# Kernel optimization log

Hardware: AMD Instinct MI355X
Metric: run time of the kernel (lower is better)

Reference implementation:

```python
import jax, jax.numpy as jnp
import numpy as np

N = 100000   # num_nodes
E = 3200000  # num_edges
F = 7        # node_features
H = 128      # hidden_dim
D = 64       # embedding_dim
EPS = 1e-5


def setup_inputs() -> dict:
    key = jax.random.key(0)
    ks = jax.random.split(key, 32)
    inp = {}
    inp["x"] = jax.random.normal(ks[0], (N, F), jnp.float32)
    inp["edge_index"] = jax.random.randint(ks[1], (2, E), 0, N, dtype=jnp.int64)
    # input projection
    inp["W_in"] = jax.random.normal(ks[2], (F, H), jnp.float32) * 0.1
    inp["b_in"] = jax.random.normal(ks[3], (H,), jnp.float32) * 0.01
    # 3 GCN layers: 128->128, 128->128, 128->64, each with eval-mode BatchNorm params
    dims = [(H, H), (H, H), (H, D)]
    for i, (di, do) in enumerate(dims):
        k = jax.random.split(ks[4 + i], 6)
        inp[f"W{i}"] = jax.random.normal(k[0], (di, do), jnp.float32) * (1.0 / np.sqrt(di))
        inp[f"b{i}"] = jax.random.normal(k[1], (do,), jnp.float32) * 0.01
        inp[f"g{i}"] = 1.0 + 0.1 * jax.random.normal(k[2], (do,), jnp.float32)
        inp[f"be{i}"] = 0.1 * jax.random.normal(k[3], (do,), jnp.float32)
        inp[f"m{i}"] = 0.1 * jax.random.normal(k[4], (do,), jnp.float32)
        inp[f"v{i}"] = jax.random.uniform(k[5], (do,), jnp.float32, 0.5, 1.5)
    return inp


def _gcn_conv(x, W, b, src, dst, dinv):
    h = x @ W                                   # [N, do]
    coef = dinv[src] * dinv[dst]                # [E]
    agg = jax.ops.segment_sum(h[src] * coef[:, None], dst, num_segments=N)
    # self-loop contribution: norm = dinv[i]^2
    return agg + h * (dinv * dinv)[:, None] + b


def _bn_eval(x, g, be, m, v):
    return (x - m) * (g * jax.lax.rsqrt(v + EPS)) + be


def reference(x, edge_index, W_in, b_in,
              W0, b0, g0, be0, m0, v0,
              W1, b1, g1, be1, m1, v1,
              W2, b2, g2, be2, m2, v2):
    src, dst = edge_index[0], edge_index[1]
    # in-degree with self-loops (same for all layers)
    deg = jax.ops.segment_sum(jnp.ones((E,), x.dtype), dst, num_segments=N) + 1.0
    dinv = jax.lax.rsqrt(deg)

    h = jax.nn.relu(x @ W_in + b_in)            # [N, H]

    # layer 0: conv -> bn -> relu -> (dropout=id, eval) -> residual
    h0 = _gcn_conv(h, W0, b0, src, dst, dinv)
    h0 = jax.nn.relu(_bn_eval(h0, g0, be0, m0, v0)) + h
    # layer 1
    h1 = _gcn_conv(h0, W1, b1, src, dst, dinv)
    h1 = jax.nn.relu(_bn_eval(h1, g1, be1, m1, v1)) + h0
    # layer 2 (final): conv -> bn only (shape changes to D, no residual/relu)
    h2 = _gcn_conv(h1, W2, b2, src, dst, dinv)
    return _bn_eval(h2, g2, be2, m2, v2)        # [N, D]
```

## Files before the change

kernel.cpp:

```cpp
#include <hip/hip_runtime.h>


#define NN 100000
#define NE 3200000
#define FI 7
#define HD 128
#define DD 64
#define EPS 1e-5f
#define NB 196
#define EPB 8192
#define NBLK ((NE + EPB - 1) / EPB)
#define EMAX 20000

typedef float float2v __attribute__((ext_vector_type(2)));
typedef short short8 __attribute__((ext_vector_type(8)));
typedef float f32x4 __attribute__((ext_vector_type(4)));

__device__ __forceinline__ unsigned char f2fp8(float f) {
    return (unsigned char)(__builtin_amdgcn_cvt_pk_fp8_f32(f, f, 0, false) & 0xFF);
}
__device__ __forceinline__ unsigned short f2bf(float f) {
    unsigned u = __float_as_uint(f);
    u += 0x7FFF + ((u >> 16) & 1);
    return (unsigned short)(u >> 16);
}


__global__ __launch_bounds__(256) void pA_bin(const int* __restrict__ ei,
                                              int* __restrict__ bcnt,
                                              int* __restrict__ ebin) {
    __shared__ int sdst[EPB];
    __shared__ int hcur[NB];
    const int t = threadIdx.x;
    for (int b = t; b < NB; b += 256) hcur[b] = 0;
    __syncthreads();
    const int base = blockIdx.x * EPB;
    const int cnt = min(EPB, NE - base);
    for (int i = t; i < cnt; i += 256) {
        int d = ei[NE + base + i];
        sdst[i] = d;
        atomicAdd(&hcur[d >> 9], 1);
    }
    __syncthreads();
    for (int b = t; b < NB; b += 256) {
        int c = hcur[b];
        hcur[b] = (c ? atomicAdd(&bcnt[b], c) : 0) + b * EMAX;
    }
    __syncthreads();
    for (int i = t; i < cnt; i += 256) {
        int s = ei[base + i];
        int d = sdst[i];
        int p = atomicAdd(&hcur[d >> 9], 1);
        ebin[p] = ((d & 511) << 23) | s;
    }
}

__global__ __launch_bounds__(512) void p4_finalize(const int* __restrict__ bcnt,
                                                   const int* __restrict__ ebin,
                                                   int* __restrict__ esrc,
                                                   int* __restrict__ rowstart,
                                                   float* __restrict__ dinv) {
    __shared__ int sh[256];
    __shared__ int lh[512];
    __shared__ int sc[512];
    __shared__ int lc[512];
    const int t = threadIdx.x;
    const int b = blockIdx.x;
    if (t < 256) sh[t] = (t < NB) ? bcnt[t] : 0;
    __syncthreads();
    for (int off = 1; off < 256; off <<= 1) {
        int v = (t < 256 && t >= off) ? sh[t - off] : 0;
        __syncthreads();
        if (t < 256) sh[t] += v;
        __syncthreads();
    }
    const int ecnt = bcnt[b];
    const int ebase = sh[b] - ecnt;
    const int rbase = b * EMAX;
    const int n0 = b << 9;
    lh[t] = 0;
    __syncthreads();
    for (int i = t; i < ecnt; i += 512)
        atomicAdd(&lh[((unsigned)ebin[rbase + i]) >> 23], 1);
    __syncthreads();
    const int c = lh[t];
    sc[t] = c;
    __syncthreads();
    for (int off = 1; off < 512; off <<= 1) {
        int v = (t >= off) ? sc[t - off] : 0;
        __syncthreads();
        sc[t] += v;
        __syncthreads();
    }
    const int excl = ebase + sc[t] - c;
    lc[t] = excl;
    const int node = n0 + t;
    if (node < NN) {
        rowstart[node] = excl;
        dinv[node] = rsqrtf((float)c + 1.0f);
    }
    if (b == NB - 1 && t == 0) rowstart[NN] = NE;
    __syncthreads();
    for (int i = t; i < ecnt; i += 512) {
        int v = ebin[rbase + i];
        int p = atomicAdd(&lc[((unsigned)v) >> 23], 1);
        esrc[p] = v & 0x7FFFFF;
    }
}


__global__ __launch_bounds__(256) void inproj_kernel(const float* __restrict__ x,
                                                     const float* __restrict__ W_in,
                                                     const float* __restrict__ b_in,
                                                     float* __restrict__ hA,
                                                     unsigned short* __restrict__ hAbf) {
    int n = blockIdx.x * 2 + (threadIdx.x >> 7);
    int j = threadIdx.x & 127;
    float acc = b_in[j];
#pragma unroll
    for (int f = 0; f < FI; ++f) acc += x[n * FI + f] * W_in[f * HD + j];
    acc = fmaxf(acc, 0.f);
    hA[n * HD + j] = acc;
    hAbf[n * HD + j] = f2bf(acc);
}


__global__ __launch_bounds__(64) void wprep_all(const float* __restrict__ W0,
                                                const float* __restrict__ W1,
                                                const float* __restrict__ W2,
                                                unsigned short* __restrict__ wf0,
                                                unsigned short* __restrict__ wf1,
                                                unsigned short* __restrict__ wf2) {
    const int blk = blockIdx.x;
    const float* W;
    unsigned short* Wf;
    int DO, rel;
    if (blk < 32) { W = W0; Wf = wf0; DO = 128; rel = blk; }
    else if (blk < 64) { W = W1; Wf = wf1; DO = 128; rel = blk - 32; }
    else { W = W2; Wf = wf2; DO = 64; rel = blk - 64; }
    const int lane = threadIdx.x;
    const int nt = rel >> 2;
    const int ks = rel & 3;
    short8 o;
#pragma unroll
    for (int j = 0; j < 8; ++j)
        o[j] = (short)f2bf(W[(ks * 32 + (lane >> 4) * 8 + j) * DO + nt * 16 + (lane & 15)]);
    *(short8*)(Wf + ((size_t)rel * 64 + lane) * 8) = o;
}


template <int DO>
__global__ __launch_bounds__(256) void gemm_mfma(const unsigned short* __restrict__ A,
                                                 const unsigned short* __restrict__ Wf,
                                                 const float* __restrict__ dinv,
                                                 unsigned char* __restrict__ B) {
    constexpr int CT = DO / 64;
    const int tid = threadIdx.x;
    const int wave = tid >> 6;
    const int lane = tid & 63;
    const int n0 = blockIdx.x * 32;
    short8 bfrag[CT][4];
#pragma unroll
    for (int ct = 0; ct < CT; ++ct)
#pragma unroll
        for (int ks = 0; ks < 4; ++ks)
            bfrag[ct][ks] = *(const short8*)(Wf + ((size_t)(((wave * CT + ct) * 4 + ks) * 64) + lane) * 8);
#pragma unroll
    for (int rt = 0; rt < 2; ++rt) {
        const int arow = n0 + rt * 16 + (lane & 15);
        short8 afrag[4];
#pragma unroll
        for (int ks = 0; ks < 4; ++ks)
            afrag[ks] = *(const short8*)(A + (size_t)arow * HD + ks * 32 + ((lane >> 4) & 3) * 8);
        f32x4 acc[CT];
#pragma unroll
        for (int ct = 0; ct < CT; ++ct) acc[ct] = (f32x4){0.f, 0.f, 0.f, 0.f};
#pragma unroll
        for (int ks = 0; ks < 4; ++ks)
#pragma unroll
            for (int ct = 0; ct < CT; ++ct)
                acc[ct] = __builtin_amdgcn_mfma_f32_16x16x32_bf16(afrag[ks], bfrag[ct][ks], acc[ct], 0, 0, 0);
#pragma unroll
        for (int r = 0; r < 4; ++r) {
            const int orow = n0 + rt * 16 + (lane >> 4) * 4 + r;
            const float dv = dinv[orow];
#pragma unroll
            for (int ct = 0; ct < CT; ++ct) {
                const int ocol = (wave * CT + ct) * 16 + (lane & 15);
                B[(size_t)orow * DO + ocol] = f2fp8(acc[ct][r] * dv);
            }
        }
    }
}


template <int DO, bool RELU_RES>
__global__ __launch_bounds__(128) void gather_kernel(const unsigned char* __restrict__ hXW,
                                                     float* __restrict__ resOut,
                                                     unsigned short* __restrict__ resBf,
                                                     const int* __restrict__ rowstart,
                                                     const int* __restrict__ esrc,
                                                     const float* __restrict__ dinv,
                                                     const float* __restrict__ bias,
                                                     const float* __restrict__ g,
                                                     const float* __restrict__ be,
                                                     const float* __restrict__ m,
                                                     const float* __restrict__ v) {
    constexpr int CG = DO / 8;
    constexpr int NG = 128 / CG;
    constexpr int QN = DO / 4;
    __shared__ int s_idx[128];
    __shared__ float sred[8][128];
    const int n = blockIdx.x;
    const int t = threadIdx.x;
    const int rs = rowstart[n];
    const int re = rowstart[n + 1];
    const float dn = dinv[n];
    const int q = t & (CG - 1);
    const int grp = t / CG;
    float4 a0l = {0.f, 0.f, 0.f, 0.f}, a0h = {0.f, 0.f, 0.f, 0.f};
    float4 a1l = {0.f, 0.f, 0.f, 0.f}, a1h = {0.f, 0.f, 0.f, 0.f};
    for (int base = rs; base < re; base += 128) {
        const int c = min(128, re - base);
        __syncthreads();
        if (t < c) s_idx[t] = esrc[base + t];
        __syncthreads();
        for (int j = grp; j < c; j += 2 * NG) {
            {
                const uint2 u = *(const uint2*)(hXW + (size_t)s_idx[j] * DO + q * 8);
                const float2v l0 = __builtin_amdgcn_cvt_pk_f32_fp8(u.x, false);
                const float2v h0 = __builtin_amdgcn_cvt_pk_f32_fp8(u.x, true);
                const float2v l1 = __builtin_amdgcn_cvt_pk_f32_fp8(u.y, false);
                const float2v h1 = __builtin_amdgcn_cvt_pk_f32_fp8(u.y, true);
                a0l.x += l0.x; a0l.y += l0.y; a0l.z += h0.x; a0l.w += h0.y;
                a0h.x += l1.x; a0h.y += l1.y; a0h.z += h1.x; a0h.w += h1.y;
            }
            if (j + NG < c) {
                const uint2 u = *(const uint2*)(hXW + (size_t)s_idx[j + NG] * DO + q * 8);
                const float2v l0 = __builtin_amdgcn_cvt_pk_f32_fp8(u.x, false);
                const float2v h0 = __builtin_amdgcn_cvt_pk_f32_fp8(u.x, true);
                const float2v l1 = __builtin_amdgcn_cvt_pk_f32_fp8(u.y, false);
                const float2v h1 = __builtin_amdgcn_cvt_pk_f32_fp8(u.y, true);
                a1l.x += l0.x; a1l.y += l0.y; a1l.z += h0.x; a1l.w += h0.y;
                a1h.x += l1.x; a1h.y += l1.y; a1h.z += h1.x; a1h.w += h1.y;
            }
        }
    }
    a0l.x += a1l.x; a0l.y += a1l.y; a0l.z += a1l.z; a0l.w += a1l.w;
    a0h.x += a1h.x; a0h.y += a1h.y; a0h.z += a1h.z; a0h.w += a1h.w;
    __syncthreads();
    sred[0][t] = a0l.x; sred[1][t] = a0l.y; sred[2][t] = a0l.z; sred[3][t] = a0l.w;
    sred[4][t] = a0h.x; sred[5][t] = a0h.y; sred[6][t] = a0h.z; sred[7][t] = a0h.w;
    __syncthreads();
    if (t < QN) {
        const int qq = t >> 1, h = t & 1;
        float4 sum = {0.f, 0.f, 0.f, 0.f};
#pragma unroll
        for (int k = 0; k < NG; ++k) {
            const int u = k * CG + qq;
            sum.x += sred[h * 4 + 0][u];
            sum.y += sred[h * 4 + 1][u];
            sum.z += sred[h * 4 + 2][u];
            sum.w += sred[h * 4 + 3][u];
        }
        const unsigned su = *(const unsigned*)(hXW + (size_t)n * DO + t * 4);
        const float2v slo = __builtin_amdgcn_cvt_pk_f32_fp8(su, false);
        const float2v shi = __builtin_amdgcn_cvt_pk_f32_fp8(su, true);
        const float4 b4 = *(const float4*)(bias + t * 4);
        const float4 g4 = *(const float4*)(g + t * 4);
        const float4 be4 = *(const float4*)(be + t * 4);
        const float4 m4 = *(const float4*)(m + t * 4);
        const float4 v4 = *(const float4*)(v + t * 4);
        float4 val;
        val.x = (sum.x + slo.x) * dn + b4.x;
        val.y = (sum.y + slo.y) * dn + b4.y;
        val.z = (sum.z + shi.x) * dn + b4.z;
        val.w = (sum.w + shi.y) * dn + b4.w;
        val.x = (val.x - m4.x) * (g4.x * rsqrtf(v4.x + EPS)) + be4.x;
        val.y = (val.y - m4.y) * (g4.y * rsqrtf(v4.y + EPS)) + be4.y;
        val.z = (val.z - m4.z) * (g4.z * rsqrtf(v4.z + EPS)) + be4.z;
        val.w = (val.w - m4.w) * (g4.w * rsqrtf(v4.w + EPS)) + be4.w;
        float4* outp = (float4*)(resOut + (size_t)n * DO + t * 4);
        if (RELU_RES) {
            const float4 r = *outp;
            val.x = fmaxf(val.x, 0.f) + r.x;
            val.y = fmaxf(val.y, 0.f) + r.y;
            val.z = fmaxf(val.z, 0.f) + r.z;
            val.w = fmaxf(val.w, 0.f) + r.w;
            ushort4 bf;
            bf.x = f2bf(val.x); bf.y = f2bf(val.y);
            bf.z = f2bf(val.z); bf.w = f2bf(val.w);
            *(ushort4*)(resBf + (size_t)n * DO + t * 4) = bf;
        }
        *outp = val;
    }
}


extern "C" void kernel_launch(void* const* d_in, const int* in_sizes, int n_in,
                              void* d_out, int out_size, void* d_ws, size_t ws_size,
                              hipStream_t stream) {
    const float* x    = (const float*)d_in[0];
    const int*   ei   = (const int*)d_in[1];
    const float* W_in = (const float*)d_in[2];
    const float* b_in = (const float*)d_in[3];
    const float* Wl[3] = {(const float*)d_in[4], (const float*)d_in[10], (const float*)d_in[16]};
    const float* bl[3] = {(const float*)d_in[5], (const float*)d_in[11], (const float*)d_in[17]};
    const float* gl[3] = {(const float*)d_in[6], (const float*)d_in[12], (const float*)d_in[18]};
    const float* bel[3] = {(const float*)d_in[7], (const float*)d_in[13], (const float*)d_in[19]};
    const float* ml[3] = {(const float*)d_in[8], (const float*)d_in[14], (const float*)d_in[20]};
    const float* vl[3] = {(const float*)d_in[9], (const float*)d_in[15], (const float*)d_in[21]};
    float* out = (float*)d_out;

    char* ws = (char*)d_ws;
    size_t off = 0;
    auto carve = [&](size_t bytes) {
        void* p = ws + off;
        off += (bytes + 255) & ~(size_t)255;
        return p;
    };
    int*   bcnt     = (int*)carve(NB * sizeof(int));
    int*   rowstart = (int*)carve((NN + 1) * sizeof(int));
    float* dinv     = (float*)carve(NN * sizeof(float));
    int*   esrc     = (int*)carve((size_t)NE * sizeof(int));
    float* hA       = (float*)carve((size_t)NN * HD * sizeof(float));
    unsigned short* hAbf = (unsigned short*)carve((size_t)NN * HD * sizeof(unsigned short));
    unsigned char* hB = (unsigned char*)carve((size_t)NN * HD);
    int*   ebin     = (int*)carve((size_t)NB * EMAX * sizeof(int));
    unsigned short* wf0 = (unsigned short*)carve((size_t)HD * HD * sizeof(unsigned short));
    unsigned short* wf1 = (unsigned short*)carve((size_t)HD * HD * sizeof(unsigned short));
    unsigned short* wf2 = (unsigned short*)carve((size_t)HD * DD * sizeof(unsigned short));
    (void)ws_size;

    hipMemsetAsync(bcnt, 0, NB * sizeof(int), stream);

    wprep_all<<<80, 64, 0, stream>>>(Wl[0], Wl[1], Wl[2], wf0, wf1, wf2);

    pA_bin<<<NBLK, 256, 0, stream>>>(ei, bcnt, ebin);
    p4_finalize<<<NB, 512, 0, stream>>>(bcnt, ebin, esrc, rowstart, dinv);

    inproj_kernel<<<NN / 2, 256, 0, stream>>>(x, W_in, b_in, hA, hAbf);

    gemm_mfma<128><<<NN / 32, 256, 0, stream>>>(hAbf, wf0, dinv, hB);
    gather_kernel<128, true><<<NN, 128, 0, stream>>>(hB, hA, hAbf, rowstart, esrc, dinv,
                                                     bl[0], gl[0], bel[0], ml[0], vl[0]);
    gemm_mfma<128><<<NN / 32, 256, 0, stream>>>(hAbf, wf1, dinv, hB);
    gather_kernel<128, true><<<NN, 128, 0, stream>>>(hB, hA, hAbf, rowstart, esrc, dinv,
                                                     bl[1], gl[1], bel[1], ml[1], vl[1]);
    gemm_mfma<64><<<NN / 32, 256, 0, stream>>>(hAbf, wf2, dinv, hB);
    gather_kernel<64, false><<<NN, 128, 0, stream>>>(hB, out, (unsigned short*)nullptr,
                                                     rowstart, esrc, dinv,
                                                     bl[2], gl[2], bel[2], ml[2], vl[2]);
}
```

Measured before the change: 516.3 us.

## Map one destination node per wavefront in gather with shuffle reduction

The CSR gather kernel used to assign one 128-thread block per node, staging edge indices in shared memory and reducing partial sums through shared memory with several block barriers. It now assigns one 64-lane wavefront per node, four nodes per 256-thread block. Each lane reads edge indices straight from global memory, and the partial sums are combined with xor shuffles, so no LDS or __syncthreads is needed. This cuts barrier and launch overhead for the roughly 32-edge average degree. In exchange each node gets fewer lanes to work in parallel, and index loads are no longer coalesced through shared memory.

After: 555.5 us. +7.6%, slower.

```diff
diff --git a/kernel.cpp b/kernel.cpp
--- a/kernel.cpp
+++ b/kernel.cpp
@@ -194,105 +194,116 @@
 }
 
 
-template <int DO, bool RELU_RES>
-__global__ __launch_bounds__(128) void gather_kernel(const unsigned char* __restrict__ hXW,
-                                                     float* __restrict__ resOut,
-                                                     unsigned short* __restrict__ resBf,
-                                                     const int* __restrict__ rowstart,
-                                                     const int* __restrict__ esrc,
-                                                     const float* __restrict__ dinv,
-                                                     const float* __restrict__ bias,
-                                                     const float* __restrict__ g,
-                                                     const float* __restrict__ be,
-                                                     const float* __restrict__ m,
-                                                     const float* __restrict__ v) {
-    constexpr int CG = DO / 8;
-    constexpr int NG = 128 / CG;
-    constexpr int QN = DO / 4;
-    __shared__ int s_idx[128];
-    __shared__ float sred[8][128];
-    const int n = blockIdx.x;
+template <int DOS, bool RELU_RES>
+__global__ __launch_bounds__(256) void gather_wave(const unsigned char* __restrict__ hXW,
+                                                   float* __restrict__ resOut,
+                                                   unsigned short* __restrict__ resBf,
+                                                   const int* __restrict__ rowstart,
+                                                   const int* __restrict__ esrc,
+                                                   const float* __restrict__ dinv,
+                                                   const float* __restrict__ bias,
+                                                   const float* __restrict__ g,
+                                                   const float* __restrict__ be,
+                                                   const float* __restrict__ m,
+                                                   const float* __restrict__ v) {
+    constexpr int CG = DOS / 8;
+    constexpr int G = 64 / CG;
     const int t = threadIdx.x;
+    const int lane = t & 63;
+    const int n = blockIdx.x * 4 + (t >> 6);
     const int rs = rowstart[n];
     const int re = rowstart[n + 1];
-    const float dn = dinv[n];
-    const int q = t & (CG - 1);
-    const int grp = t / CG;
-    float4 a0l = {0.f, 0.f, 0.f, 0.f}, a0h = {0.f, 0.f, 0.f, 0.f};
-    float4 a1l = {0.f, 0.f, 0.f, 0.f}, a1h = {0.f, 0.f, 0.f, 0.f};
-    for (int base = rs; base < re; base += 128) {
-        const int c = min(128, re - base);
-        __syncthreads();
-        if (t < c) s_idx[t] = esrc[base + t];
-        __syncthreads();
-        for (int j = grp; j < c; j += 2 * NG) {
-            {
-                const uint2 u = *(const uint2*)(hXW + (size_t)s_idx[j] * DO + q * 8);
-                const float2v l0 = __builtin_amdgcn_cvt_pk_f32_fp8(u.x, false);
-                const float2v h0 = __builtin_amdgcn_cvt_pk_f32_fp8(u.x, true);
-                const float2v l1 = __builtin_amdgcn_cvt_pk_f32_fp8(u.y, false);
-                const float2v h1 = __builtin_amdgcn_cvt_pk_f32_fp8(u.y, true);
-                a0l.x += l0.x; a0l.y += l0.y; a0l.z += h0.x; a0l.w += h0.y;
-                a0h.x += l1.x; a0h.y += l1.y; a0h.z += h1.x; a0h.w += h1.y;
-            }
-            if (j + NG < c) {
-                const uint2 u = *(const uint2*)(hXW + (size_t)s_idx[j + NG] * DO + q * 8);
-                const float2v l0 = __builtin_amdgcn_cvt_pk_f32_fp8(u.x, false);
-                const float2v h0 = __builtin_amdgcn_cvt_pk_f32_fp8(u.x, true);
-                const float2v l1 = __builtin_amdgcn_cvt_pk_f32_fp8(u.y, false);
-                const float2v h1 = __builtin_amdgcn_cvt_pk_f32_fp8(u.y, true);
-                a1l.x += l0.x; a1l.y += l0.y; a1l.z += h0.x; a1l.w += h0.y;
-                a1h.x += l1.x; a1h.y += l1.y; a1h.z += h1.x; a1h.w += h1.y;
-            }
+    const int q = lane & (CG - 1);
+    const int grp = lane / CG;
+    float4 al = {0.f, 0.f, 0.f, 0.f}, ah = {0.f, 0.f, 0.f, 0.f};
+    float4 bl = {0.f, 0.f, 0.f, 0.f}, bh = {0.f, 0.f, 0.f, 0.f};
+    for (int j = rs + grp; j < re; j += 2 * G) {
+        {
+            const int idx = esrc[j];
+            const uint2 u = *(const uint2*)(hXW + (size_t)idx * DOS + q * 8);
+            const float2v l0 = __builtin_amdgcn_cvt_pk_f32_fp8(u.x, false);
+            const float2v h0 = __builtin_amdgcn_cvt_pk_f32_fp8(u.x, true);
+            const float2v l1 = __builtin_amdgcn_cvt_pk_f32_fp8(u.y, false);
+            const float2v h1 = __builtin_amdgcn_cvt_pk_f32_fp8(u.y, true);
+            al.x += l0.x; al.y += l0.y; al.z += h0.x; al.w += h0.y;
+            ah.x += l1.x; ah.y += l1.y; ah.z += h1.x; ah.w += h1.y;
         }
-    }
-    a0l.x += a1l.x; a0l.y += a1l.y; a0l.z += a1l.z; a0l.w += a1l.w;
-    a0h.x += a1h.x; a0h.y += a1h.y; a0h.z += a1h.z; a0h.w += a1h.w;
-    __syncthreads();
-    sred[0][t] = a0l.x; sred[1][t] = a0l.y; sred[2][t] = a0l.z; sred[3][t] = a0l.w;
-    sred[4][t] = a0h.x; sred[5][t] = a0h.y; sred[6][t] = a0h.z; sred[7][t] = a0h.w;
-    __syncthreads();
-    if (t < QN) {
-        const int qq = t >> 1, h = t & 1;
-        float4 sum = {0.f, 0.f, 0.f, 0.f};
-#pragma unroll
-        for (int k = 0; k < NG; ++k) {
-            const int u = k * CG + qq;
-            sum.x += sred[h * 4 + 0][u];
-            sum.y += sred[h * 4 + 1][u];
-            sum.z += sred[h * 4 + 2][u];
-            sum.w += sred[h * 4 + 3][u];
+        if (j + G < re) {
+            const int idx = esrc[j + G];
+            const uint2 u = *(const uint2*)(hXW + (size_t)idx * DOS + q * 8);
+            const float2v l0 = __builtin_amdgcn_cvt_pk_f32_fp8(u.x, false);
+            const float2v h0 = __builtin_amdgcn_cvt_pk_f32_fp8(u.x, true);
+            const float2v l1 = __builtin_amdgcn_cvt_pk_f32_fp8(u.y, false);
+            const float2v h1 = __builtin_amdgcn_cvt_pk_f32_fp8(u.y, true);
+            bl.x += l0.x; bl.y += l0.y; bl.z += h0.x; bl.w += h0.y;
+            bh.x += l1.x; bh.y += l1.y; bh.z += h1.x; bh.w += h1.y;
         }
-        const unsigned su = *(const unsigned*)(hXW + (size_t)n * DO + t * 4);
-        const float2v slo = __builtin_amdgcn_cvt_pk_f32_fp8(su, false);
-        const float2v shi = __builtin_amdgcn_cvt_pk_f32_fp8(su, true);
-        const float4 b4 = *(const float4*)(bias + t * 4);
-        const float4 g4 = *(const float4*)(g + t * 4);
-        const float4 be4 = *(const float4*)(be + t * 4);
-        const float4 m4 = *(const float4*)(m + t * 4);
-        const float4 v4 = *(const float4*)(v + t * 4);
-        float4 val;
-        val.x = (sum.x + slo.x) * dn + b4.x;
-        val.y = (sum.y + slo.y) * dn + b4.y;
-        val.z = (sum.z + shi.x) * dn + b4.z;
-        val.w = (sum.w + shi.y) * dn + b4.w;
-        val.x = (val.x - m4.x) * (g4.x * rsqrtf(v4.x + EPS)) + be4.x;
-        val.y = (val.y - m4.y) * (g4.y * rsqrtf(v4.y + EPS)) + be4.y;
-        val.z = (val.z - m4.z) * (g4.z * rsqrtf(v4.z + EPS)) + be4.z;
-        val.w = (val.w - m4.w) * (g4.w * rsqrtf(v4.w + EPS)) + be4.w;
-        float4* outp = (float4*)(resOut + (size_t)n * DO + t * 4);
+    }
+    al.x += bl.x; al.y += bl.y; al.z += bl.z; al.w += bl.w;
+    ah.x += bh.x; ah.y += bh.y; ah.z += bh.z; ah.w += bh.w;
+#pragma unroll
+    for (int mask = CG; mask < 64; mask <<= 1) {
+        al.x += __shfl_xor(al.x, mask); al.y += __shfl_xor(al.y, mask);
+        al.z += __shfl_xor(al.z, mask); al.w += __shfl_xor(al.w, mask);
+        ah.x += __shfl_xor(ah.x, mask); ah.y += __shfl_xor(ah.y, mask);
+        ah.z += __shfl_xor(ah.z, mask); ah.w += __shfl_xor(ah.w, mask);
+    }
+    if (lane < CG) {
+        const float dn = dinv[n];
+        const uint2 su = *(const uint2*)(hXW + (size_t)n * DOS + q * 8);
+        const float2v s0l = __builtin_amdgcn_cvt_pk_f32_fp8(su.x, false);
+        const float2v s0h = __builtin_amdgcn_cvt_pk_f32_fp8(su.x, true);
+        const float2v s1l = __builtin_amdgcn_cvt_pk_f32_fp8(su.y, false);
+        const float2v s1h = __builtin_amdgcn_cvt_pk_f32_fp8(su.y, true);
+        const int c0 = q * 8;
+        const float4 b4a = *(const float4*)(bias + c0);
+        const float4 b4b = *(const float4*)(bias + c0 + 4);
+        const float4 g4a = *(const float4*)(g + c0);
+        const float4 g4b = *(const float4*)(g + c0 + 4);
+        const float4 e4a = *(const float4*)(be + c0);
+        const float4 e4b = *(const float4*)(be + c0 + 4);
+        const float4 m4a = *(const float4*)(m + c0);
+        const float4 m4b = *(const float4*)(m + c0 + 4);
+        const float4 v4a = *(const float4*)(v + c0);
+        const float4 v4b = *(const float4*)(v + c0 + 4);
+        float4 o1, o2;
+        o1.x = (al.x + s0l.x) * dn + b4a.x;
+        o1.y = (al.y + s0l.y) * dn + b4a.y;
+        o1.z = (al.z + s0h.x) * dn + b4a.z;
+        o1.w = (al.w + s0h.y) * dn + b4a.w;
+        o2.x = (ah.x + s1l.x) * dn + b4b.x;
+        o2.y = (ah.y + s1l.y) * dn + b4b.y;
+        o2.z = (ah.z + s1h.x) * dn + b4b.z;
+        o2.w = (ah.w + s1h.y) * dn + b4b.w;
+        o1.x = (o1.x - m4a.x) * (g4a.x * rsqrtf(v4a.x + EPS)) + e4a.x;
+        o1.y = (o1.y - m4a.y) * (g4a.y * rsqrtf(v4a.y + EPS)) + e4a.y;
+        o1.z = (o1.z - m4a.z) * (g4a.z * rsqrtf(v4a.z + EPS)) + e4a.z;
+        o1.w = (o1.w - m4a.w) * (g4a.w * rsqrtf(v4a.w + EPS)) + e4a.w;
+        o2.x = (o2.x - m4b.x) * (g4b.x * rsqrtf(v4b.x + EPS)) + e4b.x;
+        o2.y = (o2.y - m4b.y) * (g4b.y * rsqrtf(v4b.y + EPS)) + e4b.y;
+        o2.z = (o2.z - m4b.z) * (g4b.z * rsqrtf(v4b.z + EPS)) + e4b.z;
+        o2.w = (o2.w - m4b.w) * (g4b.w * rsqrtf(v4b.w + EPS)) + e4b.w;
+        float* outp = resOut + (size_t)n * DOS + c0;
         if (RELU_RES) {
-            const float4 r = *outp;
-            val.x = fmaxf(val.x, 0.f) + r.x;
-            val.y = fmaxf(val.y, 0.f) + r.y;
-            val.z = fmaxf(val.z, 0.f) + r.z;
-            val.w = fmaxf(val.w, 0.f) + r.w;
-            ushort4 bf;
-            bf.x = f2bf(val.x); bf.y = f2bf(val.y);
-            bf.z = f2bf(val.z); bf.w = f2bf(val.w);
-            *(ushort4*)(resBf + (size_t)n * DO + t * 4) = bf;
+            const float4 r1 = *(const float4*)outp;
+            const float4 r2 = *(const float4*)(outp + 4);
+            o1.x = fmaxf(o1.x, 0.f) + r1.x;
+            o1.y = fmaxf(o1.y, 0.f) + r1.y;
+            o1.z = fmaxf(o1.z, 0.f) + r1.z;
+            o1.w = fmaxf(o1.w, 0.f) + r1.w;
+            o2.x = fmaxf(o2.x, 0.f) + r2.x;
+            o2.y = fmaxf(o2.y, 0.f) + r2.y;
+            o2.z = fmaxf(o2.z, 0.f) + r2.z;
+            o2.w = fmaxf(o2.w, 0.f) + r2.w;
+            short8 bf;
+            bf[0] = (short)f2bf(o1.x); bf[1] = (short)f2bf(o1.y);
+            bf[2] = (short)f2bf(o1.z); bf[3] = (short)f2bf(o1.w);
+            bf[4] = (short)f2bf(o2.x); bf[5] = (short)f2bf(o2.y);
+            bf[6] = (short)f2bf(o2.z); bf[7] = (short)f2bf(o2.w);
+            *(short8*)(resBf + (size_t)n * DOS + c0) = bf;
         }
-        *outp = val;
+        *(float4*)outp = o1;
+        *(float4*)(outp + 4) = o2;
     }
 }
 
@@ -342,13 +353,13 @@
     inproj_kernel<<<NN / 2, 256, 0, stream>>>(x, W_in, b_in, hA, hAbf);
 
     gemm_mfma<128><<<NN / 32, 256, 0, stream>>>(hAbf, wf0, dinv, hB);
-    gather_kernel<128, true><<<NN, 128, 0, stream>>>(hB, hA, hAbf, rowstart, esrc, dinv,
-                                                     bl[0], gl[0], bel[0], ml[0], vl[0]);
+    gather_wave<128, true><<<NN / 4, 256, 0, stream>>>(hB, hA, hAbf, rowstart, esrc, dinv,
+                                                       bl[0], gl[0], bel[0], ml[0], vl[0]);
     gemm_mfma<128><<<NN / 32, 256, 0, stream>>>(hAbf, wf1, dinv, hB);
-    gather_kernel<128, true><<<NN, 128, 0, stream>>>(hB, hA, hAbf, rowstart, esrc, dinv,
-                                                     bl[1], gl[1], bel[1], ml[1], vl[1]);
+    gather_wave<128, true><<<NN / 4, 256, 0, stream>>>(hB, hA, hAbf, rowstart, esrc, dinv,
+                                                       bl[1], gl[1], bel[1], ml[1], vl[1]);
     gemm_mfma<64><<<NN / 32, 256, 0, stream>>>(hAbf, wf2, dinv, hB);
-    gather_kernel<64, false><<<NN, 128, 0, stream>>>(hB, out, (unsigned short*)nullptr,
-                                                     rowstart, esrc, dinv,
-                                                     bl[2], gl[2], bel[2], ml[2], vl[2]);
-}
+    gather_wave<64, false><<<NN / 4, 256, 0, stream>>>(hB, out, (unsigned short*)nullptr,
+                                                       rowstart, esrc, dinv,
+                                                       bl[2], gl[2], bel[2], ml[2], vl[2]);
+}
```
